# Kernel tuning notes

Hardware: AMD Instinct MI355X
Metric: run time of the kernel (lower is better)

## Reference

```python
import jax, jax.numpy as jnp
import numpy as np
from jax import lax

SD = 16          # sample_duration
STRIDE = 16      # feat_stride
SCALES = (4, 8, 16)
RATIOS = (0.5, 1.0, 2.0)
PRE_NMS = 1000   # proposals kept before NMS (TEST config)
POST_NMS = 128   # proposals kept after NMS
NMS_TH = 0.7


def _anchors2d():
    base = 16.0
    ctr = (base - 1.0) / 2.0
    out = []
    for r in RATIOS:
        ws = np.round(np.sqrt(base * base / r))
        hs = np.round(ws * r)
        for s in SCALES:
            w, h = ws * s, hs * s
            out.append([ctr - (w - 1) / 2, ctr - (h - 1) / 2,
                        ctr + (w - 1) / 2, ctr + (h - 1) / 2])
    return np.asarray(out, np.float32)                       # (9, 4)


def _anchors3d():
    # tube anchors: (x1, y1, t1, x2, y2, t2), durations [SD, SD/2, SD/4]
    a2 = _anchors2d()
    out = []
    for d in (SD, SD // 2, SD // 4):
        for a in a2:
            out.append([a[0], a[1], 0.0, a[2], a[3], d - 1.0])
    return np.asarray(out, np.float32)                       # (27, 6)


def _shifted(anchors, H, W):
    k = anchors.shape[-1]
    sx = jnp.arange(W, dtype=jnp.float32) * STRIDE
    sy = jnp.arange(H, dtype=jnp.float32) * STRIDE
    if k == 4:
        sh = jnp.stack(jnp.broadcast_arrays(sx[None, :], sy[:, None],
                                            sx[None, :], sy[:, None]), -1)
    else:
        z = jnp.zeros((H, W), jnp.float32)
        sh = jnp.stack(jnp.broadcast_arrays(sx[None, :], sy[:, None], z,
                                            sx[None, :], sy[:, None], z), -1)
    return (sh[:, :, None, :] + jnp.asarray(anchors)[None, None]).reshape(-1, k)


def _decode(anchors, deltas):
    # deltas layout: (d_ctr..., d_logsize...); works for 2D (k=4) and 3D (k=6)
    nd = anchors.shape[-1] // 2
    lo, hi = anchors[..., :nd], anchors[..., nd:]
    size = hi - lo + 1.0
    ctr = lo + 0.5 * (size - 1.0)
    pctr = deltas[..., :nd] * size + ctr
    psize = jnp.exp(deltas[..., nd:]) * size
    return jnp.concatenate([pctr - 0.5 * (psize - 1.0),
                            pctr + 0.5 * (psize - 1.0)], -1)


def _iou(b, boxes):
    # b: (k,), boxes: (N, k); area/volume IoU with +1 pixel convention
    nd = boxes.shape[-1] // 2
    lo = jnp.maximum(b[:nd], boxes[:, :nd])
    hi = jnp.minimum(b[nd:], boxes[:, nd:])
    inter = jnp.prod(jnp.maximum(hi - lo + 1.0, 0.0), -1)
    va = jnp.prod(b[nd:] - b[:nd] + 1.0)
    vb = jnp.prod(boxes[:, nd:] - boxes[:, :nd] + 1.0, -1)
    return inter / (va + vb - inter)


def _nms(boxes):
    # boxes already sorted by descending score; greedy NMS, fixed output size
    N = boxes.shape[0]

    def body(i, c):
        supp, keep = c
        idx = jnp.argmax(~supp)                 # first unsuppressed box
        keep = keep.at[i].set(idx.astype(jnp.int32))
        supp = supp | (_iou(boxes[idx], boxes) > NMS_TH)
        supp = supp.at[idx].set(True)
        return supp, keep

    _, keep = lax.fori_loop(0, POST_NMS, body,
                            (jnp.zeros(N, bool), jnp.zeros(POST_NMS, jnp.int32)))
    return keep


def _proposals(scores, deltas, anchors, maxs):
    # scores (B,N), deltas (B,N,k), anchors (N,k), maxs (B,1,k)
    boxes = jnp.clip(_decode(anchors[None], deltas), 0.0, maxs)
    _, idx = lax.top_k(scores, PRE_NMS)
    bx = jnp.take_along_axis(boxes, idx[..., None], axis=1)   # (B,PRE,k)
    keep = jax.vmap(_nms)(bx)                                 # (B,POST)
    sel = jnp.take_along_axis(bx, keep[..., None], axis=1)    # (B,POST,k)
    bidx = jnp.broadcast_to(
        jnp.arange(sel.shape[0], dtype=sel.dtype)[:, None, None],
        sel.shape[:2] + (1,))
    return lax.stop_gradient(jnp.concatenate([bidx, sel], -1))


def setup_inputs() -> dict:
    k = jax.random.split(jax.random.key(0), 8)
    s = 0.01
    return {
        "base_feat": jax.random.normal(k[0], (1, 256, 16, 32, 32), jnp.float32),
        "im_info": jnp.array([[512.0, 512.0, 1.0]], jnp.float32),
        "gt_boxes": jax.random.uniform(k[1], (1, 5, 7), jnp.float32) * 100.0,
        "gt_rois": jax.random.uniform(k[2], (1, 5, 16, 5), jnp.float32) * 100.0,
        "W_conv": jax.random.normal(k[3], (512, 256, 3, 3, 3), jnp.float32) * s,
        "b_conv": jnp.zeros((512,), jnp.float32),
        "W_cls": jax.random.normal(k[4], (54, 512), jnp.float32) * s,
        "b_cls": jnp.zeros((54,), jnp.float32),
        "W_bbox": jax.random.normal(k[5], (162, 512), jnp.float32) * s,
        "b_bbox": jnp.zeros((162,), jnp.float32),
        "W_cls16": jax.random.normal(k[6], (18, 512), jnp.float32) * s,
        "b_cls16": jnp.zeros((18,), jnp.float32),
        "W_bbox16": jax.random.normal(k[7], (36, 512), jnp.float32) * s,
        "b_bbox16": jnp.zeros((36,), jnp.float32),
    }


def reference(base_feat, im_info, gt_boxes, gt_rois, W_conv, b_conv,
              W_cls, b_cls, W_bbox, b_bbox, W_cls16, b_cls16,
              W_bbox16, b_bbox16):
    B, _, T, H, W = base_feat.shape
    # RPN_Conv: 3x3x3 Conv3d + ReLU
    conv1 = jax.nn.relu(
        lax.conv_general_dilated(base_feat, W_conv, (1, 1, 1), "SAME",
                                 dimension_numbers=("NCDHW", "OIDHW", "NCDHW"))
        + b_conv[None, :, None, None, None])
    # 1x1x1 score / bbox heads (3D)
    cls3 = jnp.einsum("bcthw,oc->bothw", conv1, W_cls) + b_cls[None, :, None, None, None]
    bbox3 = jnp.einsum("bcthw,oc->bothw", conv1, W_bbox) + b_bbox[None, :, None, None, None]
    # permute(0,1,3,4,2).mean(4) == mean over the temporal axis
    feat2 = conv1.mean(axis=2)
    cls2 = jnp.einsum("bchw,oc->bohw", feat2, W_cls16) + b_cls16[None, :, None, None]
    bbox2 = jnp.einsum("bchw,oc->bohw", feat2, W_bbox16) + b_bbox16[None, :, None, None]
    # reshape(x,2) + softmax over dim 1; fg prob is the second half of channels
    fg3 = jax.nn.softmax(cls3.reshape(B, 2, 27, T, H, W), axis=1)[:, 1]  # (B,27,T,H,W)
    fg2 = jax.nn.softmax(cls2.reshape(B, 2, 9, H, W), axis=1)[:, 1]      # (B,9,H,W)
    # proposal layers consume detached tensors (torch .data)
    fg3, fg2, bbox3d, bbox2d = map(lax.stop_gradient, (fg3, fg2, bbox3, bbox2))
    # flatten position-major (h, w, anchor)
    sc3 = fg3.mean(axis=2).transpose(0, 2, 3, 1).reshape(B, -1)
    dl3 = bbox3d.mean(axis=2).reshape(B, 27, 6, H, W).transpose(0, 3, 4, 1, 2).reshape(B, -1, 6)
    sc2 = fg2.transpose(0, 2, 3, 1).reshape(B, -1)
    dl2 = bbox2d.reshape(B, 9, 4, H, W).transpose(0, 3, 4, 1, 2).reshape(B, -1, 4)
    imh, imw = im_info[:, 0][:, None], im_info[:, 1][:, None]
    sdm = jnp.full_like(imw, SD - 1.0)
    max3 = jnp.stack([imw - 1, imh - 1, sdm, imw - 1, imh - 1, sdm], -1)  # (B,1,6)
    max2 = jnp.stack([imw - 1, imh - 1, imw - 1, imh - 1], -1)            # (B,1,4)
    rois = _proposals(sc3, dl3, _shifted(_anchors3d(), H, W), max3)       # (B,POST,7)
    rois16 = _proposals(sc2, dl2, _shifted(_anchors2d(), H, W), max2)     # (B,POST,5)
    z = jnp.zeros((), jnp.float32)  # eval mode: all RPN losses are 0
    return rois, rois16, z, z, z, z
```

## Files before the change

### kernel.cpp

```cpp
#include <hip/hip_runtime.h>
#include <hip/hip_bf16.h>
#include <cfloat>
#include <cstdint>


#define T_DIM 16
#define H_DIM 32
#define W_DIM 32
#define NVOX  (T_DIM*H_DIM*W_DIM)
#define HW    (H_DIM*W_DIM)
#define CIN   256
#define COUT  512
#define PRE_NMS 1000
#define POST_NMS 128
#define NMS_TH 0.7f

typedef __attribute__((ext_vector_type(8))) short v8s;
typedef __attribute__((ext_vector_type(4))) float v4f;
typedef __attribute__((ext_vector_type(4))) int v4i;

#define MFMA_B16(A,B,C) __builtin_amdgcn_mfma_f32_16x16x32_bf16(A,B,C,0,0,0)

__device__ __forceinline__ short f2bf(float x) {
    unsigned u = __float_as_uint(x);
    u += 0x7FFFu + ((u >> 16) & 1u);
    return (short)(u >> 16);
}
__device__ __forceinline__ float bf2f(short s) {
    return __uint_as_float(((unsigned)(unsigned short)s) << 16);
}

__constant__ float c_ws[3] = {23.f, 16.f, 11.f};
__constant__ float c_hs[3] = {12.f, 16.f, 22.f};
__constant__ float c_sc[3] = {4.f, 8.f, 16.f};
__constant__ float c_depth[3] = {16.f, 8.f, 4.f};

__global__ void k_split_w(const float* __restrict__ W, short* __restrict__ A0,
                          short* __restrict__ A1, short* __restrict__ A2) {
    int i = blockIdx.x * 256 + threadIdx.x;
    int c7 = i & 7;
    int o = (i >> 3) & 511;
    int ko = (i >> 12) & 31;
    int tap = i >> 17;
    int c = ko * 8 + c7;
    float x = W[(o * 256 + c) * 27 + tap];
    short h = f2bf(x); float r = x - bf2f(h);
    short m = f2bf(r); float r2 = r - bf2f(m);
    short l = f2bf(r2);
    A0[i] = h; A1[i] = m; A2[i] = l;
}

__global__ void k_build_wcomb(const float* __restrict__ Wcls, const float* __restrict__ Wbb,
                              float* __restrict__ Wc) {
    int i = blockIdx.x * 256 + threadIdx.x;
    int o = i & 255;
    int c = i >> 8;
    float v = 0.f;
    if (o < 54) v = Wcls[o * 512 + c];
    else if (o < 216) v = Wbb[(o - 54) * 512 + c];
    Wc[i] = v;
}

#define SPLIT2(X0, X1, OH, OM, OL) {                                          \
    unsigned u0_ = __float_as_uint(X0), u1_ = __float_as_uint(X1);            \
    OH = (int)__builtin_amdgcn_perm(u1_, u0_, 0x07060302u);                   \
    float h0_ = __uint_as_float(u0_ & 0xFFFF0000u);                           \
    float h1_ = __uint_as_float(u1_ & 0xFFFF0000u);                           \
    float r0_ = (X0) - h0_, r1_ = (X1) - h1_;                                 \
    unsigned v0_ = __float_as_uint(r0_), v1_ = __float_as_uint(r1_);          \
    OM = (int)__builtin_amdgcn_perm(v1_, v0_, 0x07060302u);                   \
    float m0_ = __uint_as_float(v0_ & 0xFFFF0000u);                           \
    float m1_ = __uint_as_float(v1_ & 0xFFFF0000u);                           \
    float s0_ = r0_ - m0_, s1_ = r1_ - m1_;                                   \
    OL = (int)__builtin_amdgcn_perm(__float_as_uint(s1_),                     \
                                    __float_as_uint(s0_), 0x07060302u);       \
}

#define CV_SHIFT(TAP) {                                                       \
    int kt_ = (TAP) / 9 - 1, kh_ = ((TAP) / 3) % 3 - 1, kw_ = (TAP) % 3 - 1;  \
    int tt_ = bt + kt_, hh_ = bh + kh_, ww_ = bw + kw_;                       \
    bVal = ((unsigned)tt_ < 16u) && ((unsigned)hh_ < 32u) && ((unsigned)ww_ < 32u); \
    bOff = bVal ? ((tt_ << 10) + (hh_ << 5) + ww_) : 0;                       \
}

#define CV_LOAD_B_RAW(CK) {                                                   \
    const float* ip_ = I + ((size_t)((CK) + skq * 8) << 14) + bOff;           \
    bx0 = bVal ? ip_[0]       : 0.f;                                          \
    bx1 = bVal ? ip_[1 << 14] : 0.f;                                          \
    bx2 = bVal ? ip_[2 << 14] : 0.f;                                          \
    bx3 = bVal ? ip_[3 << 14] : 0.f;                                          \
    bx4 = bVal ? ip_[4 << 14] : 0.f;                                          \
    bx5 = bVal ? ip_[5 << 14] : 0.f;                                          \
    bx6 = bVal ? ip_[6 << 14] : 0.f;                                          \
    bx7 = bVal ? ip_[7 << 14] : 0.f;                                          \
}

#define CV_SPLIT_B() {                                                        \
    int h01,h23,h45,h67,m01,m23,m45,m67,l01,l23,l45,l67;                      \
    SPLIT2(bx0, bx1, h01, m01, l01);                                          \
    SPLIT2(bx2, bx3, h23, m23, l23);                                          \
    SPLIT2(bx4, bx5, h45, m45, l45);                                          \
    SPLIT2(bx6, bx7, h67, m67, l67);                                          \
    pbh0 = (v4i){h01, h23, h45, h67};                                         \
    pbm0 = (v4i){m01, m23, m45, m67};                                         \
    pbl0 = (v4i){l01, l23, l45, l67};                                         \
}

#define LOAD_ASET(S) {                                                        \
    const size_t aB_ = (((size_t)((S) >> 3) * 32 + (((S) & 7) << 2)) << 12) + aLane; \
    ah0 = *(const v8s*)(A0 + aB_); ah1 = *(const v8s*)(A0 + aB_ + 128);       \
    am0 = *(const v8s*)(A1 + aB_); am1 = *(const v8s*)(A1 + aB_ + 128);       \
    al0 = *(const v8s*)(A2 + aB_); al1 = *(const v8s*)(A2 + aB_ + 128);       \
}

#define COMPUTE() {                                                           \
    _Pragma("unroll")                                                         \
    for (int j = 0; j < 4; ++j) {                                             \
        v8s bb = *(const v8s*)(&Bsh[0][uB + j * 16]);                         \
        v8s bm = *(const v8s*)(&Bsh[1][uB + j * 16]);                         \
        v8s bl = *(const v8s*)(&Bsh[2][uB + j * 16]);                         \
        v4f a;                                                                \
        a = acc[0][j];                                                        \
        a = MFMA_B16(ah0, bb, a); a = MFMA_B16(ah0, bm, a);                   \
        a = MFMA_B16(am0, bb, a); a = MFMA_B16(ah0, bl, a);                   \
        a = MFMA_B16(am0, bm, a); a = MFMA_B16(al0, bb, a);                   \
        acc[0][j] = a;                                                        \
        a = acc[1][j];                                                        \
        a = MFMA_B16(ah1, bb, a); a = MFMA_B16(ah1, bm, a);                   \
        a = MFMA_B16(am1, bb, a); a = MFMA_B16(ah1, bl, a);                   \
        a = MFMA_B16(am1, bm, a); a = MFMA_B16(al1, bb, a);                   \
        acc[1][j] = a;                                                        \
    }                                                                         \
}

__global__ __launch_bounds__(512, 4) void k_conv3d_mfma(
        const float* __restrict__ I, const short* __restrict__ A0,
        const short* __restrict__ A1, const short* __restrict__ A2,
        const float* __restrict__ bias, float* __restrict__ O) {
    __shared__ v4i Bsh[3][512];
    const int tid = threadIdx.x;
    const int o0 = blockIdx.y * 128;
    const int v0 = blockIdx.x * 128;
    const int lane = tid & 63;
    const int wv = tid >> 6;
    const int quad = lane >> 4, m16 = lane & 15;
    const int wo = (wv >> 1) * 32;
    const int wvx = (wv & 1) * 64;

    const int sa_o = tid >> 2, skq = tid & 3;
    const int uW = skq * 128 + sa_o;

    const int vbase = v0 + sa_o;
    const int bt = vbase >> 10, bh = (vbase >> 5) & 31, bw = vbase & 31;

    const int uB = quad * 128 + wvx + m16;

    const size_t aLane = ((size_t)(o0 + wo + m16) << 3) + ((size_t)quad << 12);

    v4f acc[2][4];
#pragma unroll
    for (int i = 0; i < 2; i++)
#pragma unroll
        for (int j = 0; j < 4; j++) acc[i][j] = (v4f){0.f, 0.f, 0.f, 0.f};

    int bOff, bVal;
    v4i pbh0, pbm0, pbl0;
    v8s ah0, ah1, am0, am1, al0, al1;
    float bx0, bx1, bx2, bx3, bx4, bx5, bx6, bx7;

    CV_SHIFT(0);
    CV_LOAD_B_RAW(0);
    CV_SPLIT_B();

    for (int s = 0; s < 216; ++s) {
        __syncthreads();
        Bsh[0][uW] = pbh0;
        Bsh[1][uW] = pbm0;
        Bsh[2][uW] = pbl0;
        __syncthreads();
        LOAD_ASET(s);
        {
            int s1 = s + 1;
            if (s1 < 216) {
                if ((s1 & 7) == 0) CV_SHIFT(s1 >> 3);
                CV_LOAD_B_RAW((s1 & 7) << 5);
            }
        }
        COMPUTE();
        if (s + 1 < 216) CV_SPLIT_B();
    }

#pragma unroll
    for (int i = 0; i < 2; ++i) {
#pragma unroll
        for (int r = 0; r < 4; ++r) {
            int o = o0 + wo + i * 16 + quad * 4 + r;
            float bo = bias[o];
            float* dst = O + (size_t)o * NVOX + v0 + wvx + m16;
#pragma unroll
            for (int j = 0; j < 4; ++j)
                dst[j * 16] = fmaxf(acc[i][j][r] + bo, 0.f);
        }
    }
}

__global__ __launch_bounds__(256) void k_gemm_logits3(const float* __restrict__ conv1,
                                                      const float* __restrict__ Wc,
                                                      float* __restrict__ L) {
    __shared__ float As[16][64];
    __shared__ float Bs[16][64];
    const int tid = threadIdx.x;
    const int o0 = blockIdx.y * 64;
    const int v0 = blockIdx.x * 64;
    const int ty = tid >> 4, tx = tid & 15;
    const int c_l = tid >> 4, e4 = (tid & 15) << 2;

    float acc[4][4];
#pragma unroll
    for (int i = 0; i < 4; i++)
#pragma unroll
        for (int j = 0; j < 4; j++) acc[i][j] = 0.f;

    for (int ck = 0; ck < 512; ck += 16) {
        __syncthreads();
        *(float4*)(&As[c_l][e4]) = *(const float4*)(Wc + ((size_t)(ck + c_l) << 8) + o0 + e4);
        *(float4*)(&Bs[c_l][e4]) = *(const float4*)(conv1 + ((size_t)(ck + c_l) << 14) + v0 + e4);
        __syncthreads();
#pragma unroll
        for (int k = 0; k < 16; ++k) {
            float a[4], b[4];
            *(float4*)(a) = *(const float4*)(&As[k][ty * 4]);
            *(float4*)(b) = *(const float4*)(&Bs[k][tx * 4]);
#pragma unroll
            for (int i = 0; i < 4; i++)
#pragma unroll
                for (int j = 0; j < 4; j++)
                    acc[i][j] = fmaf(a[i], b[j], acc[i][j]);
        }
    }
#pragma unroll
    for (int i = 0; i < 4; i++) {
        float* dst = L + (size_t)(o0 + ty * 4 + i) * NVOX + v0 + tx * 4;
        *(float4*)(dst) = *(const float4*)(&acc[i][0]);
    }
}

__global__ void k_sc3(const float* __restrict__ L, const float* __restrict__ b_cls,
                      float* __restrict__ sc3) {
    int i = blockIdx.x * 256 + threadIdx.x;
    if (i >= 27 * HW) return;
    int a = i >> 10, hw = i & 1023;
    float b0 = b_cls[a], b1 = b_cls[27 + a];
    const float* L0 = L + (size_t)a * NVOX + hw;
    const float* L1 = L + (size_t)(27 + a) * NVOX + hw;
    float s = 0.f;
    for (int t = 0; t < T_DIM; t++) {
        float x0 = L0[t * HW] + b0, x1 = L1[t * HW] + b1;
        float m = fmaxf(x0, x1);
        float e0 = expf(x0 - m), e1 = expf(x1 - m);
        s += e1 / (e0 + e1);
    }
    sc3[hw * 27 + a] = s * (1.f / 16.f);
}

__global__ void k_dl3(const float* __restrict__ L, const float* __restrict__ b_bbox,
                      float* __restrict__ dl3) {
    int i = blockIdx.x * 256 + threadIdx.x;
    if (i >= 162 * HW) return;
    int ch = i >> 10, hw = i & 1023;
    const float* Lr = L + (size_t)(54 + ch) * NVOX + hw;
    float s = 0.f;
    for (int t = 0; t < T_DIM; t++) s += Lr[t * HW];
    s = s * (1.f / 16.f) + b_bbox[ch];
    int a = ch / 6, d = ch - a * 6;
    dl3[((size_t)hw * 27 + a) * 6 + d] = s;
}

__global__ void k_feat2(const float* __restrict__ conv1, float* __restrict__ feat2) {
    int i = blockIdx.x * 256 + threadIdx.x;
    int c = i >> 10, hw = i & 1023;
    const float* src = conv1 + (size_t)c * NVOX + hw;
    float s = 0.f;
    for (int t = 0; t < T_DIM; t++) s += src[t * HW];
    feat2[i] = s * (1.f / 16.f);
}

__global__ void k_gemm2d(const float* __restrict__ feat2, const float* __restrict__ Wcls16,
                         const float* __restrict__ Wbb16, float* __restrict__ L2) {
    int g = blockIdx.x * 256 + threadIdx.x;
    int o = g >> 10, hw = g & 1023;
    const float* wrow = (o < 18) ? (Wcls16 + (size_t)o * 512) : (Wbb16 + (size_t)(o - 18) * 512);
    float s = 0.f;
    for (int c = 0; c < 512; c++) s = fmaf(wrow[c], feat2[(size_t)c * HW + hw], s);
    L2[(size_t)o * HW + hw] = s;
}

__global__ void k_sc2(const float* __restrict__ L2, const float* __restrict__ b_cls16,
                      float* __restrict__ sc2) {
    int i = blockIdx.x * 256 + threadIdx.x;
    if (i >= 9 * HW) return;
    int a = i >> 10, hw = i & 1023;
    float x0 = L2[(size_t)a * HW + hw] + b_cls16[a];
    float x1 = L2[(size_t)(9 + a) * HW + hw] + b_cls16[9 + a];
    float m = fmaxf(x0, x1);
    float e0 = expf(x0 - m), e1 = expf(x1 - m);
    sc2[hw * 9 + a] = e1 / (e0 + e1);
}

__global__ void k_dl2(const float* __restrict__ L2, const float* __restrict__ b_bbox16,
                      float* __restrict__ dl2) {
    int i = blockIdx.x * 256 + threadIdx.x;
    if (i >= 36 * HW) return;
    int ch = i >> 10, hw = i & 1023;
    float v = L2[(size_t)(18 + ch) * HW + hw] + b_bbox16[ch];
    int a = ch >> 2, d = ch & 3;
    dl2[((size_t)hw * 9 + a) * 4 + d] = v;
}

__device__ __forceinline__ unsigned mapf(float f) {
    unsigned u = __float_as_uint(f);
    return (u & 0x80000000u) ? ~u : (u | 0x80000000u);
}

__global__ __launch_bounds__(1024) void k_proposal(const float* __restrict__ im_info,
                                                   const float* __restrict__ sc3,
                                                   const float* __restrict__ dl3,
                                                   const float* __restrict__ sc2,
                                                   const float* __restrict__ dl2,
                                                   float* __restrict__ out) {
    const int branch = blockIdx.x;
    const int tid = threadIdx.x;
    const int A = (branch == 0) ? 27 : 9;
    const int nd = (branch == 0) ? 3 : 2;
    const float* scores = (branch == 0) ? sc3 : sc2;
    const float* deltas = (branch == 0) ? dl3 : dl2;
    const int K = PRE_NMS;
    const int ept = A;
    const int base = tid * ept;

    __shared__ unsigned hist[256];
    __shared__ unsigned long long keys[1024];
    __shared__ float bx[PRE_NMS][6];
    __shared__ int keep[POST_NMS];
    __shared__ unsigned wsum[16];
    __shared__ unsigned long long alive[16];
    __shared__ int sh_b, sh_next, bcast;

    unsigned prefix = 0;
    int rank = K;
    for (int shift = 24; shift >= 0; shift -= 8) {
        if (tid < 256) hist[tid] = 0;
        __syncthreads();
        const unsigned mask_hi = (shift == 24) ? 0u : (0xFFFFFFFFu << (shift + 8));
        for (int j = 0; j < ept; j++) {
            unsigned m = mapf(scores[base + j]);
            if ((m & mask_hi) == prefix)
                atomicAdd(&hist[(m >> shift) & 255], 1u);
        }
        __syncthreads();
        for (int d = 1; d < 256; d <<= 1) {
            unsigned add = 0;
            if (tid < 256 && tid + d < 256) add = hist[tid + d];
            __syncthreads();
            if (tid < 256) hist[tid] += add;
            __syncthreads();
        }
        if (tid < 256) {
            bool win = (hist[tid] >= (unsigned)rank) &&
                       (tid == 255 || hist[tid + 1] < (unsigned)rank);
            if (win) { sh_b = tid; sh_next = (tid == 255) ? 0 : (int)hist[tid + 1]; }
        }
        __syncthreads();
        prefix |= (unsigned)sh_b << shift;
        rank -= sh_next;
        __syncthreads();
    }
    const unsigned tau = prefix;

    int gt_c = 0, eq_c = 0;
    for (int j = 0; j < ept; j++) {
        unsigned m = mapf(scores[base + j]);
        gt_c += (m > tau);
        eq_c += (m == tau);
    }
    unsigned cnt = ((unsigned)gt_c << 16) | (unsigned)eq_c;
    const int lane = tid & 63, wid = tid >> 6;
    unsigned x = cnt;
    for (int d = 1; d < 64; d <<= 1) {
        unsigned y = __shfl_up(x, d);
        if (lane >= d) x += y;
    }
    if (lane == 63) wsum[wid] = x;
    __syncthreads();
    if (wid == 0) {
        unsigned w = (lane < 16) ? wsum[lane] : 0;
        for (int d = 1; d < 16; d <<= 1) {
            unsigned y = __shfl_up(w, d);
            if (lane >= d) w += y;
        }
        if (lane < 16) wsum[lane] = w;
    }
    __syncthreads();
    unsigned excl = x - cnt + (wid ? wsum[wid - 1] : 0);
    const int c1 = (int)(wsum[15] >> 16);
    int gi = (int)(excl >> 16);
    int ei = (int)(excl & 0xFFFFu);
    for (int j = 0; j < ept; j++) {
        int idx = base + j;
        unsigned m = mapf(scores[idx]);
        unsigned long long key = ((unsigned long long)m << 32) |
                                 (unsigned)(0xFFFFFFFFu - (unsigned)idx);
        if (m > tau) {
            keys[gi++] = key;
        } else if (m == tau) {
            if (c1 + ei < K) keys[c1 + ei] = key;
            ei++;
        }
    }
    if (tid < 1024 - K) keys[K + tid] = 0;
    __syncthreads();

    for (int k = 2; k <= 1024; k <<= 1) {
        for (int j = k >> 1; j > 0; j >>= 1) {
            int ixj = tid ^ j;
            if (ixj > tid) {
                unsigned long long a = keys[tid], b = keys[ixj];
                bool sw2 = ((tid & k) == 0) ? (a < b) : (a > b);
                if (sw2) { keys[tid] = b; keys[ixj] = a; }
            }
            __syncthreads();
        }
    }

    const float imh = im_info[0], imw = im_info[1];
    if (tid < K) {
        int n = (int)(0xFFFFFFFFu - (unsigned)(keys[tid] & 0xFFFFFFFFull));
        int cell = n / A, a = n - cell * A;
        int hc = cell >> 5, wc = cell & 31;
        int a2 = (branch == 0) ? (a % 9) : a;
        int ri = a2 / 3, si = a2 % 3;
        float w = c_ws[ri] * c_sc[si], h = c_hs[ri] * c_sc[si];
        float lo[3], hi[3], mx[3];
        lo[0] = 7.5f - (w - 1.f) * 0.5f + 16.f * wc;
        hi[0] = 7.5f + (w - 1.f) * 0.5f + 16.f * wc;
        mx[0] = imw - 1.f;
        lo[1] = 7.5f - (h - 1.f) * 0.5f + 16.f * hc;
        hi[1] = 7.5f + (h - 1.f) * 0.5f + 16.f * hc;
        mx[1] = imh - 1.f;
        if (branch == 0) { lo[2] = 0.f; hi[2] = c_depth[a / 9] - 1.f; mx[2] = (float)(T_DIM - 1); }
        const float* dp = deltas + (size_t)n * (2 * nd);
        for (int d = 0; d < nd; d++) {
            float size = hi[d] - lo[d] + 1.f;
            float ctr = lo[d] + 0.5f * (size - 1.f);
            float pctr = dp[d] * size + ctr;
            float psize = expf(dp[nd + d]) * size;
            float pl = pctr - 0.5f * (psize - 1.f);
            float ph = pctr + 0.5f * (psize - 1.f);
            bx[tid][d]      = fminf(fmaxf(pl, 0.f), mx[d]);
            bx[tid][nd + d] = fminf(fmaxf(ph, 0.f), mx[d]);
        }
    }
    if (tid < 16) alive[tid] = (tid < 15) ? ~0ull : ((1ull << (K - 15 * 64)) - 1);
    __syncthreads();

    float myb[6]; float myvol = 1.f;
    if (tid < K) {
        for (int d = 0; d < 6; d++) myb[d] = bx[tid][d];
        for (int d = 0; d < nd; d++) myvol *= (myb[nd + d] - myb[d] + 1.f);
    }
    for (int i = 0; i < POST_NMS; ++i) {
        if (tid < 64) {
            unsigned long long wvb = (tid < 16) ? alive[tid] : 0ull;
            int cand = wvb ? (tid * 64 + __ffsll(wvb) - 1) : 0x7fffffff;
#pragma unroll
            for (int off = 32; off; off >>= 1)
                cand = min(cand, __shfl_xor(cand, off));
            if (tid == 0) {
                int m = (cand == 0x7fffffff) ? 0 : cand;
                bcast = m; keep[i] = m;
            }
        }
        __syncthreads();
        int sel = bcast;
        bool s = false;
        if (tid < K) {
            float inter = 1.f, selvol = 1.f;
            for (int d = 0; d < nd; d++) {
                float slo = bx[sel][d], shi = bx[sel][nd + d];
                float l = fmaxf(slo, myb[d]);
                float hh = fminf(shi, myb[nd + d]);
                inter *= fmaxf(hh - l + 1.f, 0.f);
                selvol *= (shi - slo + 1.f);
            }
            float iou = inter / (selvol + myvol - inter);
            s = (iou > NMS_TH) || (tid == sel);
        }
        unsigned long long bal = __ballot(s);
        if (lane == 0 && bal) alive[wid] &= ~bal;
        __syncthreads();
    }

    if (tid < POST_NMS) {
        int k = keep[tid];
        if (branch == 0) {
            float* o = out + (size_t)tid * 7;
            o[0] = 0.f;
            for (int d = 0; d < 6; d++) o[1 + d] = bx[k][d];
        } else {
            float* o = out + 128 * 7 + (size_t)tid * 5;
            o[0] = 0.f;
            for (int d = 0; d < 4; d++) o[1 + d] = bx[k][d];
        }
    }
    if (branch == 0 && tid == 0) {
        out[1536] = 0.f; out[1537] = 0.f; out[1538] = 0.f; out[1539] = 0.f;
    }
}

extern "C" void kernel_launch(void* const* d_in, const int* in_sizes, int n_in,
                              void* d_out, int out_size, void* d_ws, size_t ws_size,
                              hipStream_t stream) {
    (void)in_sizes; (void)n_in; (void)out_size; (void)ws_size;
    const float* base_feat = (const float*)d_in[0];
    const float* im_info   = (const float*)d_in[1];
    const float* W_conv    = (const float*)d_in[4];
    const float* b_conv    = (const float*)d_in[5];
    const float* W_cls     = (const float*)d_in[6];
    const float* b_cls     = (const float*)d_in[7];
    const float* W_bbox    = (const float*)d_in[8];
    const float* b_bbox    = (const float*)d_in[9];
    const float* W_cls16   = (const float*)d_in[10];
    const float* b_cls16   = (const float*)d_in[11];
    const float* W_bbox16  = (const float*)d_in[12];
    const float* b_bbox16  = (const float*)d_in[13];
    float* out = (float*)d_out;

    char* ws = (char*)d_ws;
    const size_t AW = (size_t)27 * 512 * 256;
    short* A0 = (short*)ws;
    short* A1 = A0 + AW;
    short* A2 = A1 + AW;
    float* L3 = (float*)ws;
    size_t off = AW * 3 * sizeof(short);
    float* Wcomb  = (float*)(ws + off); off += (size_t)512 * 256 * 4;
    float* conv1  = (float*)(ws + off); off += (size_t)COUT * NVOX * 4;
    float* feat2  = (float*)(ws + off); off += (size_t)512 * HW * 4;
    float* L2     = (float*)(ws + off); off += (size_t)64 * HW * 4;
    float* sc3    = (float*)(ws + off); off += (size_t)27 * HW * 4;
    float* dl3    = (float*)(ws + off); off += (size_t)27 * HW * 6 * 4;
    float* sc2    = (float*)(ws + off); off += (size_t)9 * HW * 4;
    float* dl2    = (float*)(ws + off); off += (size_t)9 * HW * 4 * 4;

    k_split_w<<<13824, 256, 0, stream>>>(W_conv, A0, A1, A2);
    k_build_wcomb<<<512, 256, 0, stream>>>(W_cls, W_bbox, Wcomb);
    {
        dim3 g(NVOX / 128, COUT / 128);
        k_conv3d_mfma<<<g, 512, 0, stream>>>(base_feat, A0, A1, A2, b_conv, conv1);
    }
    {
        dim3 g(NVOX / 64, 4);
        k_gemm_logits3<<<g, 256, 0, stream>>>(conv1, Wcomb, L3);
    }
    k_sc3<<<(27 * HW + 255) / 256, 256, 0, stream>>>(L3, b_cls, sc3);
    k_dl3<<<(162 * HW + 255) / 256, 256, 0, stream>>>(L3, b_bbox, dl3);
    k_feat2<<<(512 * HW) / 256, 256, 0, stream>>>(conv1, feat2);
    k_gemm2d<<<(54 * HW) / 256, 256, 0, stream>>>(feat2, W_cls16, W_bbox16, L2);
    k_sc2<<<(9 * HW + 255) / 256, 256, 0, stream>>>(L2, b_cls16, sc2);
    k_dl2<<<(36 * HW + 255) / 256, 256, 0, stream>>>(L2, b_bbox16, dl2);
    k_proposal<<<2, 1024, 0, stream>>>(im_info, sc3, dl3, sc2, dl2, out);
}
```

Before: 988.6 us.

## Pre-split conv input into bf16 triplets and double per-wave output tile

Adds a pre-pass kernel that splits the fp32 input features into hi/mid/lo bf16 parts once, so the conv kernel loads packed vectors instead of re-splitting each voxel for every tap. The conv block drops from 512 to 256 threads, with each wave computing 64 output channels instead of 32, which doubles A-fragment register reuse per shared B tile. This costs extra workspace memory and triples input bandwidth through the pre-split buffers, and raises register pressure (16 accumulators plus 12 A fragments), which may lower occupancy.

```diff
diff --git a/kernel.cpp b/kernel.cpp
--- a/kernel.cpp
+++ b/kernel.cpp
@@ -76,6 +76,24 @@
                                     __float_as_uint(s0_), 0x07060302u);       \
 }
 
+__global__ void k_split_i(const float* __restrict__ I, v4i* __restrict__ Ih,
+                          v4i* __restrict__ Im, v4i* __restrict__ Il) {
+    int t = blockIdx.x * 256 + threadIdx.x;
+    int vox = t & 16383;
+    int ck8 = t >> 14;
+    const float* ip = I + ((size_t)ck8 << 3) * NVOX + vox;
+    int h[4], m[4], l[4];
+#pragma unroll
+    for (int j = 0; j < 4; ++j) {
+        float x0 = ip[(size_t)(2 * j) * NVOX];
+        float x1 = ip[(size_t)(2 * j + 1) * NVOX];
+        SPLIT2(x0, x1, h[j], m[j], l[j]);
+    }
+    Ih[t] = (v4i){h[0], h[1], h[2], h[3]};
+    Im[t] = (v4i){m[0], m[1], m[2], m[3]};
+    Il[t] = (v4i){l[0], l[1], l[2], l[3]};
+}
+
 #define CV_SHIFT(TAP) {                                                       \
     int kt_ = (TAP) / 9 - 1, kh_ = ((TAP) / 3) % 3 - 1, kw_ = (TAP) % 3 - 1;  \
     int tt_ = bt + kt_, hh_ = bh + kh_, ww_ = bw + kw_;                       \
@@ -83,34 +101,28 @@
     bOff = bVal ? ((tt_ << 10) + (hh_ << 5) + ww_) : 0;                       \
 }
 
-#define CV_LOAD_B_RAW(CK) {                                                   \
-    const float* ip_ = I + ((size_t)((CK) + skq * 8) << 14) + bOff;           \
-    bx0 = bVal ? ip_[0]       : 0.f;                                          \
-    bx1 = bVal ? ip_[1 << 14] : 0.f;                                          \
-    bx2 = bVal ? ip_[2 << 14] : 0.f;                                          \
-    bx3 = bVal ? ip_[3 << 14] : 0.f;                                          \
-    bx4 = bVal ? ip_[4 << 14] : 0.f;                                          \
-    bx5 = bVal ? ip_[5 << 14] : 0.f;                                          \
-    bx6 = bVal ? ip_[6 << 14] : 0.f;                                          \
-    bx7 = bVal ? ip_[7 << 14] : 0.f;                                          \
-}
-
-#define CV_SPLIT_B() {                                                        \
-    int h01,h23,h45,h67,m01,m23,m45,m67,l01,l23,l45,l67;                      \
-    SPLIT2(bx0, bx1, h01, m01, l01);                                          \
-    SPLIT2(bx2, bx3, h23, m23, l23);                                          \
-    SPLIT2(bx4, bx5, h45, m45, l45);                                          \
-    SPLIT2(bx6, bx7, h67, m67, l67);                                          \
-    pbh0 = (v4i){h01, h23, h45, h67};                                         \
-    pbm0 = (v4i){m01, m23, m45, m67};                                         \
-    pbl0 = (v4i){l01, l23, l45, l67};                                         \
+#define CV_LOAD_BP(CK8B) {                                                    \
+    const size_t bidx_ = (((size_t)((CK8B) + skh * 2)) << 14) + bOff;         \
+    nh0 = Ih[bidx_]; nh1 = Ih[bidx_ + NVOX];                                  \
+    nm0 = Im[bidx_]; nm1 = Im[bidx_ + NVOX];                                  \
+    nl0 = Il[bidx_]; nl1 = Il[bidx_ + NVOX];                                  \
+}
+
+#define CV_SELECT_B() {                                                       \
+    v4i z_ = (v4i){0, 0, 0, 0};                                               \
+    pbh0 = bVal ? nh0 : z_; pbh1 = bVal ? nh1 : z_;                           \
+    pbm0 = bVal ? nm0 : z_; pbm1 = bVal ? nm1 : z_;                           \
+    pbl0 = bVal ? nl0 : z_; pbl1 = bVal ? nl1 : z_;                           \
 }
 
 #define LOAD_ASET(S) {                                                        \
     const size_t aB_ = (((size_t)((S) >> 3) * 32 + (((S) & 7) << 2)) << 12) + aLane; \
-    ah0 = *(const v8s*)(A0 + aB_); ah1 = *(const v8s*)(A0 + aB_ + 128);       \
-    am0 = *(const v8s*)(A1 + aB_); am1 = *(const v8s*)(A1 + aB_ + 128);       \
-    al0 = *(const v8s*)(A2 + aB_); al1 = *(const v8s*)(A2 + aB_ + 128);       \
+    ah0 = *(const v8s*)(A0 + aB_);       ah1 = *(const v8s*)(A0 + aB_ + 128); \
+    ah2 = *(const v8s*)(A0 + aB_ + 256); ah3 = *(const v8s*)(A0 + aB_ + 384); \
+    am0 = *(const v8s*)(A1 + aB_);       am1 = *(const v8s*)(A1 + aB_ + 128); \
+    am2 = *(const v8s*)(A1 + aB_ + 256); am3 = *(const v8s*)(A1 + aB_ + 384); \
+    al0 = *(const v8s*)(A2 + aB_);       al1 = *(const v8s*)(A2 + aB_ + 128); \
+    al2 = *(const v8s*)(A2 + aB_ + 256); al3 = *(const v8s*)(A2 + aB_ + 384); \
 }
 
 #define COMPUTE() {                                                           \
@@ -130,11 +142,22 @@
         a = MFMA_B16(am1, bb, a); a = MFMA_B16(ah1, bl, a);                   \
         a = MFMA_B16(am1, bm, a); a = MFMA_B16(al1, bb, a);                   \
         acc[1][j] = a;                                                        \
+        a = acc[2][j];                                                        \
+        a = MFMA_B16(ah2, bb, a); a = MFMA_B16(ah2, bm, a);                   \
+        a = MFMA_B16(am2, bb, a); a = MFMA_B16(ah2, bl, a);                   \
+        a = MFMA_B16(am2, bm, a); a = MFMA_B16(al2, bb, a);                   \
+        acc[2][j] = a;                                                        \
+        a = acc[3][j];                                                        \
+        a = MFMA_B16(ah3, bb, a); a = MFMA_B16(ah3, bm, a);                   \
+        a = MFMA_B16(am3, bb, a); a = MFMA_B16(ah3, bl, a);                   \
+        a = MFMA_B16(am3, bm, a); a = MFMA_B16(al3, bb, a);                   \
+        acc[3][j] = a;                                                        \
     }                                                                         \
 }
 
-__global__ __launch_bounds__(512, 4) void k_conv3d_mfma(
-        const float* __restrict__ I, const short* __restrict__ A0,
+__global__ __launch_bounds__(256) void k_conv3d_mfma(
+        const v4i* __restrict__ Ih, const v4i* __restrict__ Im,
+        const v4i* __restrict__ Il, const short* __restrict__ A0,
         const short* __restrict__ A1, const short* __restrict__ A2,
         const float* __restrict__ bias, float* __restrict__ O) {
     __shared__ v4i Bsh[3][512];
@@ -144,11 +167,12 @@
     const int lane = tid & 63;
     const int wv = tid >> 6;
     const int quad = lane >> 4, m16 = lane & 15;
-    const int wo = (wv >> 1) * 32;
+    const int wo = (wv >> 1) * 64;
     const int wvx = (wv & 1) * 64;
 
-    const int sa_o = tid >> 2, skq = tid & 3;
-    const int uW = skq * 128 + sa_o;
+    const int sa_o = tid >> 1, skh = tid & 1;
+    const int uW0 = (skh * 2) * 128 + sa_o;
+    const int uW1 = (skh * 2 + 1) * 128 + sa_o;
 
     const int vbase = v0 + sa_o;
     const int bt = vbase >> 10, bh = (vbase >> 5) & 31, bw = vbase & 31;
@@ -157,41 +181,41 @@
 
     const size_t aLane = ((size_t)(o0 + wo + m16) << 3) + ((size_t)quad << 12);
 
-    v4f acc[2][4];
-#pragma unroll
-    for (int i = 0; i < 2; i++)
+    v4f acc[4][4];
+#pragma unroll
+    for (int i = 0; i < 4; i++)
 #pragma unroll
         for (int j = 0; j < 4; j++) acc[i][j] = (v4f){0.f, 0.f, 0.f, 0.f};
 
     int bOff, bVal;
-    v4i pbh0, pbm0, pbl0;
-    v8s ah0, ah1, am0, am1, al0, al1;
-    float bx0, bx1, bx2, bx3, bx4, bx5, bx6, bx7;
+    v4i pbh0, pbh1, pbm0, pbm1, pbl0, pbl1;
+    v4i nh0, nh1, nm0, nm1, nl0, nl1;
+    v8s ah0, ah1, ah2, ah3, am0, am1, am2, am3, al0, al1, al2, al3;
 
     CV_SHIFT(0);
-    CV_LOAD_B_RAW(0);
-    CV_SPLIT_B();
+    CV_LOAD_BP(0);
+    CV_SELECT_B();
 
     for (int s = 0; s < 216; ++s) {
         __syncthreads();
-        Bsh[0][uW] = pbh0;
-        Bsh[1][uW] = pbm0;
-        Bsh[2][uW] = pbl0;
+        Bsh[0][uW0] = pbh0; Bsh[0][uW1] = pbh1;
+        Bsh[1][uW0] = pbm0; Bsh[1][uW1] = pbm1;
+        Bsh[2][uW0] = pbl0; Bsh[2][uW1] = pbl1;
         __syncthreads();
         LOAD_ASET(s);
         {
             int s1 = s + 1;
             if (s1 < 216) {
                 if ((s1 & 7) == 0) CV_SHIFT(s1 >> 3);
-                CV_LOAD_B_RAW((s1 & 7) << 5);
+                CV_LOAD_BP((s1 & 7) << 2);
             }
         }
         COMPUTE();
-        if (s + 1 < 216) CV_SPLIT_B();
-    }
-
-#pragma unroll
-    for (int i = 0; i < 2; ++i) {
+        if (s + 1 < 216) CV_SELECT_B();
+    }
+
+#pragma unroll
+    for (int i = 0; i < 4; ++i) {
 #pragma unroll
         for (int r = 0; r < 4; ++r) {
             int o = o0 + wo + i * 16 + quad * 4 + r;
@@ -550,12 +574,16 @@
     float* dl3    = (float*)(ws + off); off += (size_t)27 * HW * 6 * 4;
     float* sc2    = (float*)(ws + off); off += (size_t)9 * HW * 4;
     float* dl2    = (float*)(ws + off); off += (size_t)9 * HW * 4 * 4;
+    v4i* Ih = (v4i*)(ws + off); off += (size_t)32 * NVOX * 16;
+    v4i* Im_ = (v4i*)(ws + off); off += (size_t)32 * NVOX * 16;
+    v4i* Il = (v4i*)(ws + off); off += (size_t)32 * NVOX * 16;
 
     k_split_w<<<13824, 256, 0, stream>>>(W_conv, A0, A1, A2);
     k_build_wcomb<<<512, 256, 0, stream>>>(W_cls, W_bbox, Wcomb);
+    k_split_i<<<2048, 256, 0, stream>>>(base_feat, Ih, Im_, Il);
     {
         dim3 g(NVOX / 128, COUT / 128);
-        k_conv3d_mfma<<<g, 512, 0, stream>>>(base_feat, A0, A1, A2, b_conv, conv1);
+        k_conv3d_mfma<<<g, 256, 0, stream>>>(Ih, Im_, Il, A0, A1, A2, b_conv, conv1);
     }
     {
         dim3 g(NVOX / 64, 4);
```

New measurement: 950.1 us. 1.04x faster.
